# Optimization experiments

Measured on AMD Instinct MI355X. Metric: run time of the kernel, lower is better.

The kernel has to match this reference:

```python
import jax, jax.numpy as jnp
import numpy as np


def _det3x3(m):
    # faithful translation of batch_det_3x3 (column-expansion form)
    return (m[..., 0, 0] * m[..., 1, 1] * m[..., 2, 2]
            + m[..., 1, 0] * m[..., 2, 1] * m[..., 0, 2]
            + m[..., 2, 0] * m[..., 1, 2] * m[..., 0, 1]
            - m[..., 0, 2] * m[..., 1, 1] * m[..., 2, 0]
            - m[..., 1, 2] * m[..., 2, 1] * m[..., 0, 0]
            - m[..., 2, 2] * m[..., 1, 0] * m[..., 0, 1])


def setup_inputs() -> dict:
    key = jax.random.key(0)
    k1, k2 = jax.random.split(key)
    B, C = 32768, 256
    x = jax.random.normal(k1, (B, C, 3, 3), dtype=jnp.float32)
    W = jax.random.normal(k2, (C,), dtype=jnp.float32) * (1.0 / np.sqrt(C))
    return {"x": x, "W": W}


def reference(x, W):
    # 1x1 conv with single output channel, no bias -> contraction over C
    camera = jnp.einsum('bchw,c->bhw', x, W)  # [B, 3, 3]
    # SVD-based orthonormalization. torch.svd returns V with A = U S V^T;
    # jnp.linalg.svd returns Vh = V^T, so torch's u @ v.transpose == u @ vh.
    u, s, vh = jnp.linalg.svd(camera, full_matrices=False)
    orth = jnp.matmul(u, vh)  # [B, 3, 3]
    # reflection fix: flip last column of U by det(orth) (+-1), recompose
    det = _det3x3(orth)  # [B]
    u_flip = jnp.concatenate([u[..., :2], u[..., 2:3] * det[:, None, None]], axis=-1)
    return jnp.matmul(u_flip, vh)
```

## Files before the change

### kernel.cpp

```cpp
#include <hip/hip_runtime.h>

__global__ __launch_bounds__(256) void camera_reduce_kernel(
    const float* __restrict__ x, const float* __restrict__ W,
    float* __restrict__ cam, int B)
{
    const int wave = threadIdx.x >> 6;
    const int lane = threadIdx.x & 63;
    const int b = blockIdx.x * 4 + wave;
    if (b >= B) return;

    const float4* xv = reinterpret_cast<const float4*>(
        x + (size_t)b * 2304 + (size_t)lane * 36);
    const float4 wv = reinterpret_cast<const float4*>(W)[lane];

    float a0 = 0.f, a1 = 0.f, a2 = 0.f, a3 = 0.f, a4 = 0.f,
          a5 = 0.f, a6 = 0.f, a7 = 0.f, a8 = 0.f;
    float4 v;
    v = xv[0]; a0 += v.x*wv.x; a1 += v.y*wv.x; a2 += v.z*wv.x; a3 += v.w*wv.x;
    v = xv[1]; a4 += v.x*wv.x; a5 += v.y*wv.x; a6 += v.z*wv.x; a7 += v.w*wv.x;
    v = xv[2]; a8 += v.x*wv.x; a0 += v.y*wv.y; a1 += v.z*wv.y; a2 += v.w*wv.y;
    v = xv[3]; a3 += v.x*wv.y; a4 += v.y*wv.y; a5 += v.z*wv.y; a6 += v.w*wv.y;
    v = xv[4]; a7 += v.x*wv.y; a8 += v.y*wv.y; a0 += v.z*wv.z; a1 += v.w*wv.z;
    v = xv[5]; a2 += v.x*wv.z; a3 += v.y*wv.z; a4 += v.z*wv.z; a5 += v.w*wv.z;
    v = xv[6]; a6 += v.x*wv.z; a7 += v.y*wv.z; a8 += v.z*wv.z; a0 += v.w*wv.w;
    v = xv[7]; a1 += v.x*wv.w; a2 += v.y*wv.w; a3 += v.z*wv.w; a4 += v.w*wv.w;
    v = xv[8]; a5 += v.x*wv.w; a6 += v.y*wv.w; a7 += v.z*wv.w; a8 += v.w*wv.w;

    #pragma unroll
    for (int m = 32; m >= 1; m >>= 1) {
        a0 += __shfl_xor(a0, m, 64);
        a1 += __shfl_xor(a1, m, 64);
        a2 += __shfl_xor(a2, m, 64);
        a3 += __shfl_xor(a3, m, 64);
        a4 += __shfl_xor(a4, m, 64);
        a5 += __shfl_xor(a5, m, 64);
        a6 += __shfl_xor(a6, m, 64);
        a7 += __shfl_xor(a7, m, 64);
        a8 += __shfl_xor(a8, m, 64);
    }

    if (lane < 9) {
        float r = (lane == 0) ? a0 : (lane == 1) ? a1 : (lane == 2) ? a2 :
                  (lane == 3) ? a3 : (lane == 4) ? a4 : (lane == 5) ? a5 :
                  (lane == 6) ? a6 : (lane == 7) ? a7 : a8;
        cam[(size_t)b * 9 + lane] = r;
    }
}

#define JROT(P, Q)                                                         \
  do {                                                                     \
    float apq = A[P][Q];                                                   \
    if (fabsf(apq) > 1e-20f) {                                             \
      float app = A[P][P], aqq = A[Q][Q];                                  \
      float tau = (aqq - app) / (2.0f * apq);                              \
      float tt = copysignf(1.0f, tau) /                                    \
                 (fabsf(tau) + sqrtf(tau * tau + 1.0f));                   \
      float c = rsqrtf(tt * tt + 1.0f);                                    \
      float s = tt * c;                                                    \
      _Pragma("unroll") for (int k = 0; k < 4; ++k) {                      \
        float t1 = A[k][P], t2 = A[k][Q];                                  \
        A[k][P] = c * t1 - s * t2;                                         \
        A[k][Q] = s * t1 + c * t2;                                         \
      }                                                                    \
      _Pragma("unroll") for (int k = 0; k < 4; ++k) {                      \
        float t1 = A[P][k], t2 = A[Q][k];                                  \
        A[P][k] = c * t1 - s * t2;                                         \
        A[Q][k] = s * t1 + c * t2;                                         \
      }                                                                    \
      _Pragma("unroll") for (int k = 0; k < 4; ++k) {                      \
        float t1 = V[k][P], t2 = V[k][Q];                                  \
        V[k][P] = c * t1 - s * t2;                                         \
        V[k][Q] = s * t1 + c * t2;                                         \
      }                                                                    \
    }                                                                      \
  } while (0)

__global__ __launch_bounds__(256) void polar_so3_kernel(float* __restrict__ io,
                                                        int B)
{
    const int t = blockIdx.x * blockDim.x + threadIdx.x;
    if (t >= B) return;
    float* p = io + (size_t)t * 9;
    const float m00 = p[0], m01 = p[1], m02 = p[2];
    const float m10 = p[3], m11 = p[4], m12 = p[5];
    const float m20 = p[6], m21 = p[7], m22 = p[8];

    float A[4][4];
    A[0][0] = m00 + m11 + m22;
    A[1][1] = m00 - m11 - m22;
    A[2][2] = m11 - m00 - m22;
    A[3][3] = m22 - m00 - m11;
    A[0][1] = A[1][0] = m21 - m12;
    A[0][2] = A[2][0] = m02 - m20;
    A[0][3] = A[3][0] = m10 - m01;
    A[1][2] = A[2][1] = m01 + m10;
    A[1][3] = A[3][1] = m02 + m20;
    A[2][3] = A[3][2] = m12 + m21;

    float V[4][4] = {{1.f, 0.f, 0.f, 0.f},
                     {0.f, 1.f, 0.f, 0.f},
                     {0.f, 0.f, 1.f, 0.f},
                     {0.f, 0.f, 0.f, 1.f}};

    #pragma unroll
    for (int sweep = 0; sweep < 5; ++sweep) {
        JROT(0, 1); JROT(0, 2); JROT(0, 3);
        JROT(1, 2); JROT(1, 3); JROT(2, 3);
    }

    int best = 0;
    float bd = A[0][0];
    if (A[1][1] > bd) { bd = A[1][1]; best = 1; }
    if (A[2][2] > bd) { bd = A[2][2]; best = 2; }
    if (A[3][3] > bd) { bd = A[3][3]; best = 3; }
    float qw = (best == 0) ? V[0][0] : (best == 1) ? V[0][1] : (best == 2) ? V[0][2] : V[0][3];
    float qx = (best == 0) ? V[1][0] : (best == 1) ? V[1][1] : (best == 2) ? V[1][2] : V[1][3];
    float qy = (best == 0) ? V[2][0] : (best == 1) ? V[2][1] : (best == 2) ? V[2][2] : V[2][3];
    float qz = (best == 0) ? V[3][0] : (best == 1) ? V[3][1] : (best == 2) ? V[3][2] : V[3][3];

    const float nrm = rsqrtf(qw * qw + qx * qx + qy * qy + qz * qz);
    qw *= nrm; qx *= nrm; qy *= nrm; qz *= nrm;

    const float xx = qx * qx, yy = qy * qy, zz = qz * qz;
    const float xy = qx * qy, xz = qx * qz, yz = qy * qz;
    const float wx = qw * qx, wy = qw * qy, wz = qw * qz;

    p[0] = 1.0f - 2.0f * (yy + zz);
    p[1] = 2.0f * (xy - wz);
    p[2] = 2.0f * (xz + wy);
    p[3] = 2.0f * (xy + wz);
    p[4] = 1.0f - 2.0f * (xx + zz);
    p[5] = 2.0f * (yz - wx);
    p[6] = 2.0f * (yz + wx) * 0.0f + 2.0f * (xz - wy);
    p[7] = 2.0f * (yz + wx);
    p[8] = 1.0f - 2.0f * (xx + yy);
}

extern "C" void kernel_launch(void* const* d_in, const int* in_sizes, int n_in,
                              void* d_out, int out_size, void* d_ws, size_t ws_size,
                              hipStream_t stream)
{
    const float* x = (const float*)d_in[0];
    const float* W = (const float*)d_in[1];
    float* out = (float*)d_out;

    const int C = in_sizes[1];
    const int B = in_sizes[0] / (C * 9);

    camera_reduce_kernel<<<(B + 3) / 4, 256, 0, stream>>>(x, W, out, B);
    polar_so3_kernel<<<(B + 255) / 256, 256, 0, stream>>>(out, B);
}
```

Before: 401.7 us.

## Coalesce x loads through LDS staging and process several batches per wave

Each wave now loads one batch element's 2304 floats with fully coalesced float4 loads (lane-contiguous), stages them in shared memory, and then reads the strided per-lane 36-float slices from LDS for the reduction. Each wave handles eight batch elements in a loop, which cuts the grid size and reuses the W load. The kernel is bound by memory bandwidth, and the old per-lane strided float4 reads were partly uncoalesced. The cost is 36 KB of LDS per block, which may limit occupancy, plus an LDS read pattern with a stride of 9 float4 that can cause bank conflicts. Loads inside the loop are serialized per element, which reduces memory-level parallelism.

```diff
diff --git a/kernel.cpp b/kernel.cpp
--- a/kernel.cpp
+++ b/kernel.cpp
@@ -1,49 +1,64 @@
 #include <hip/hip_runtime.h>
 
+constexpr int WAVES_PER_BLOCK = 4;
+constexpr int BS_PER_WAVE = 8;
+
 __global__ __launch_bounds__(256) void camera_reduce_kernel(
-    const float* __restrict__ x, const float* __restrict__ W,
+    const float4* __restrict__ x4, const float* __restrict__ W,
     float* __restrict__ cam, int B)
 {
+    __shared__ float4 tile[WAVES_PER_BLOCK][576];
     const int wave = threadIdx.x >> 6;
     const int lane = threadIdx.x & 63;
-    const int b = blockIdx.x * 4 + wave;
-    if (b >= B) return;
+    const int wave_id = blockIdx.x * WAVES_PER_BLOCK + wave;
+    const float4 wv = reinterpret_cast<const float4*>(W)[lane];
+    float4* my = tile[wave];
 
-    const float4* xv = reinterpret_cast<const float4*>(
-        x + (size_t)b * 2304 + (size_t)lane * 36);
-    const float4 wv = reinterpret_cast<const float4*>(W)[lane];
+    const int b0 = wave_id * BS_PER_WAVE;
+    for (int i = 0; i < BS_PER_WAVE; ++i) {
+        const int b = b0 + i;
+        if (b >= B) break;
 
-    float a0 = 0.f, a1 = 0.f, a2 = 0.f, a3 = 0.f, a4 = 0.f,
-          a5 = 0.f, a6 = 0.f, a7 = 0.f, a8 = 0.f;
-    float4 v;
-    v = xv[0]; a0 += v.x*wv.x; a1 += v.y*wv.x; a2 += v.z*wv.x; a3 += v.w*wv.x;
-    v = xv[1]; a4 += v.x*wv.x; a5 += v.y*wv.x; a6 += v.z*wv.x; a7 += v.w*wv.x;
-    v = xv[2]; a8 += v.x*wv.x; a0 += v.y*wv.y; a1 += v.z*wv.y; a2 += v.w*wv.y;
-    v = xv[3]; a3 += v.x*wv.y; a4 += v.y*wv.y; a5 += v.z*wv.y; a6 += v.w*wv.y;
-    v = xv[4]; a7 += v.x*wv.y; a8 += v.y*wv.y; a0 += v.z*wv.z; a1 += v.w*wv.z;
-    v = xv[5]; a2 += v.x*wv.z; a3 += v.y*wv.z; a4 += v.z*wv.z; a5 += v.w*wv.z;
-    v = xv[6]; a6 += v.x*wv.z; a7 += v.y*wv.z; a8 += v.z*wv.z; a0 += v.w*wv.w;
-    v = xv[7]; a1 += v.x*wv.w; a2 += v.y*wv.w; a3 += v.z*wv.w; a4 += v.w*wv.w;
-    v = xv[8]; a5 += v.x*wv.w; a6 += v.y*wv.w; a7 += v.z*wv.w; a8 += v.w*wv.w;
+        const float4* src = x4 + (size_t)b * 576 + lane;
+        float4 r[9];
+        #pragma unroll
+        for (int k = 0; k < 9; ++k) r[k] = src[(size_t)k * 64];
 
-    #pragma unroll
-    for (int m = 32; m >= 1; m >>= 1) {
-        a0 += __shfl_xor(a0, m, 64);
-        a1 += __shfl_xor(a1, m, 64);
-        a2 += __shfl_xor(a2, m, 64);
-        a3 += __shfl_xor(a3, m, 64);
-        a4 += __shfl_xor(a4, m, 64);
-        a5 += __shfl_xor(a5, m, 64);
-        a6 += __shfl_xor(a6, m, 64);
-        a7 += __shfl_xor(a7, m, 64);
-        a8 += __shfl_xor(a8, m, 64);
-    }
+        #pragma unroll
+        for (int k = 0; k < 9; ++k) my[lane + 64 * k] = r[k];
 
-    if (lane < 9) {
-        float r = (lane == 0) ? a0 : (lane == 1) ? a1 : (lane == 2) ? a2 :
-                  (lane == 3) ? a3 : (lane == 4) ? a4 : (lane == 5) ? a5 :
-                  (lane == 6) ? a6 : (lane == 7) ? a7 : a8;
-        cam[(size_t)b * 9 + lane] = r;
+        float a0 = 0.f, a1 = 0.f, a2 = 0.f, a3 = 0.f, a4 = 0.f,
+              a5 = 0.f, a6 = 0.f, a7 = 0.f, a8 = 0.f;
+        float4 v;
+        v = my[9*lane+0]; a0 += v.x*wv.x; a1 += v.y*wv.x; a2 += v.z*wv.x; a3 += v.w*wv.x;
+        v = my[9*lane+1]; a4 += v.x*wv.x; a5 += v.y*wv.x; a6 += v.z*wv.x; a7 += v.w*wv.x;
+        v = my[9*lane+2]; a8 += v.x*wv.x; a0 += v.y*wv.y; a1 += v.z*wv.y; a2 += v.w*wv.y;
+        v = my[9*lane+3]; a3 += v.x*wv.y; a4 += v.y*wv.y; a5 += v.z*wv.y; a6 += v.w*wv.y;
+        v = my[9*lane+4]; a7 += v.x*wv.y; a8 += v.y*wv.y; a0 += v.z*wv.z; a1 += v.w*wv.z;
+        v = my[9*lane+5]; a2 += v.x*wv.z; a3 += v.y*wv.z; a4 += v.z*wv.z; a5 += v.w*wv.z;
+        v = my[9*lane+6]; a6 += v.x*wv.z; a7 += v.y*wv.z; a8 += v.z*wv.z; a0 += v.w*wv.w;
+        v = my[9*lane+7]; a1 += v.x*wv.w; a2 += v.y*wv.w; a3 += v.z*wv.w; a4 += v.w*wv.w;
+        v = my[9*lane+8]; a5 += v.x*wv.w; a6 += v.y*wv.w; a7 += v.z*wv.w; a8 += v.w*wv.w;
+
+        #pragma unroll
+        for (int m = 32; m >= 1; m >>= 1) {
+            a0 += __shfl_xor(a0, m, 64);
+            a1 += __shfl_xor(a1, m, 64);
+            a2 += __shfl_xor(a2, m, 64);
+            a3 += __shfl_xor(a3, m, 64);
+            a4 += __shfl_xor(a4, m, 64);
+            a5 += __shfl_xor(a5, m, 64);
+            a6 += __shfl_xor(a6, m, 64);
+            a7 += __shfl_xor(a7, m, 64);
+            a8 += __shfl_xor(a8, m, 64);
+        }
+
+        if (lane < 9) {
+            float out = (lane == 0) ? a0 : (lane == 1) ? a1 : (lane == 2) ? a2 :
+                        (lane == 3) ? a3 : (lane == 4) ? a4 : (lane == 5) ? a5 :
+                        (lane == 6) ? a6 : (lane == 7) ? a7 : a8;
+            cam[(size_t)b * 9 + lane] = out;
+        }
     }
 }
 
@@ -131,7 +146,7 @@
     p[3] = 2.0f * (xy + wz);
     p[4] = 1.0f - 2.0f * (xx + zz);
     p[5] = 2.0f * (yz - wx);
-    p[6] = 2.0f * (yz + wx) * 0.0f + 2.0f * (xz - wy);
+    p[6] = 2.0f * (xz - wy);
     p[7] = 2.0f * (yz + wx);
     p[8] = 1.0f - 2.0f * (xx + yy);
 }
@@ -147,6 +162,10 @@
     const int C = in_sizes[1];
     const int B = in_sizes[0] / (C * 9);
 
-    camera_reduce_kernel<<<(B + 3) / 4, 256, 0, stream>>>(x, W, out, B);
+    const int waves_needed = (B + BS_PER_WAVE - 1) / BS_PER_WAVE;
+    const int blocks = (waves_needed + WAVES_PER_BLOCK - 1) / WAVES_PER_BLOCK;
+
+    camera_reduce_kernel<<<blocks, 256, 0, stream>>>(
+        (const float4*)x, W, out, B);
     polar_so3_kernel<<<(B + 255) / 256, 256, 0, stream>>>(out, B);
 }
```

Result: slower. 411.7 us (+2.5%).
